# Performance work log

Measured on AMD Instinct MI355X. Metric: run time of the kernel, lower is better.

## Reference

```python
import jax, jax.numpy as jnp
import numpy as np

H = 16
D_MODEL = 1024
D_K = D_MODEL // H


def setup_inputs() -> dict:
    key = jax.random.key(0)
    ks = jax.random.split(key, 12)
    B, S = 4, 2048
    scale = 1.0 / np.sqrt(D_MODEL)
    inp = {
        "query": jax.random.normal(ks[0], (B, S, D_MODEL), dtype=jnp.float32),
        "key": jax.random.normal(ks[1], (B, S, D_MODEL), dtype=jnp.float32),
        "value": jax.random.normal(ks[2], (B, S, D_MODEL), dtype=jnp.float32),
        "Wq": jax.random.normal(ks[3], (D_MODEL, D_MODEL), dtype=jnp.float32) * scale,
        "bq": jnp.zeros((D_MODEL,), dtype=jnp.float32),
        "Wk": jax.random.normal(ks[4], (D_MODEL, D_MODEL), dtype=jnp.float32) * scale,
        "bk": jnp.zeros((D_MODEL,), dtype=jnp.float32),
        "Wv": jax.random.normal(ks[5], (D_MODEL, D_MODEL), dtype=jnp.float32) * scale,
        "bv": jnp.zeros((D_MODEL,), dtype=jnp.float32),
        "Wo": jax.random.normal(ks[6], (D_MODEL, D_MODEL), dtype=jnp.float32) * scale,
        "bo": jnp.zeros((D_MODEL,), dtype=jnp.float32),
    }
    return inp


def reference(query, key, value, Wq, bq, Wk, bk, Wv, bv, Wo, bo):
    B, S, _ = query.shape
    # Linear projections (torch Linear: x @ W^T + b), then split heads -> [B,H,S,d_k]
    def proj(x, W, b):
        y = x @ W.T + b
        return y.reshape(B, S, H, D_K).transpose(0, 2, 1, 3)

    q = proj(query, Wq, bq)
    k = proj(key, Wk, bk)
    v = proj(value, Wv, bv)

    # Explicit QK^T / sqrt(d_k), softmax, AV (no mask; dropout = identity in eval)
    scores = jnp.einsum("bhqd,bhkd->bhqk", q, k) / jnp.sqrt(jnp.float32(D_K))
    attn = jax.nn.softmax(scores, axis=-1)
    x = jnp.einsum("bhqk,bhkd->bhqd", attn, v)

    # Merge heads and final output projection
    x = x.transpose(0, 2, 1, 3).reshape(B, S, H * D_K)
    return x @ Wo.T + bo
```

## Files before the change

### kernel.cpp

```cpp
#include <hip/hip_runtime.h>
#include <hip/hip_bf16.h>
#include <stdint.h>

#define BATCH 4
#define SEQ   2048
#define DM    1024
#define NH    16
#define DK    64
#define MROWS (BATCH * SEQ)

#define C1 0.1803368801111204f

typedef __attribute__((ext_vector_type(8))) short short8;
typedef __attribute__((ext_vector_type(4))) float f32x4;
typedef __attribute__((ext_vector_type(4))) float floatv4;
typedef __attribute__((ext_vector_type(4))) unsigned short us4;
typedef __attribute__((ext_vector_type(4))) unsigned int uint4v;

static __device__ __forceinline__ unsigned short f2bf(float f) {
    union { float f; uint32_t u; } c; c.f = f;
    uint32_t u = c.u;
    return (unsigned short)((u + 0x7fffu + ((u >> 16) & 1u)) >> 16);
}

static __device__ __forceinline__ unsigned int cvt_pk_bf16(float a, float b) {
    __hip_bfloat162 h = __float22bfloat162_rn(float2{a, b});
    unsigned int u; __builtin_memcpy(&u, &h, 4); return u;
}

static __device__ __forceinline__ float ex2(float x) { return __builtin_amdgcn_exp2f(x); }

#define AS1C(p) ((const __attribute__((address_space(1))) unsigned int*)(uintptr_t)(const void*)(p))
#define AS3(p)  ((__attribute__((address_space(3))) unsigned int*)(uintptr_t)(void*)(p))

__global__ __launch_bounds__(256) void cvt3_k(const float* __restrict__ a, const float* __restrict__ b,
                                              const float* __restrict__ c,
                                              unsigned short* __restrict__ oa, unsigned short* __restrict__ ob,
                                              unsigned short* __restrict__ oc) {
    const int z = blockIdx.y;
    const float* s = (z == 0) ? a : (z == 1) ? b : c;
    unsigned short* o = (z == 0) ? oa : (z == 1) ? ob : oc;
    int i = blockIdx.x * 256 + threadIdx.x;
    floatv4 v = ((const floatv4*)s)[i];
    us4 w; w.x = f2bf(v.x); w.y = f2bf(v.y); w.z = f2bf(v.z); w.w = f2bf(v.w);
    ((us4*)o)[i] = w;
}

__global__ __launch_bounds__(256) void cvt4_k(const float* __restrict__ a, const float* __restrict__ b,
                                              const float* __restrict__ c, const float* __restrict__ d,
                                              unsigned short* __restrict__ oa, unsigned short* __restrict__ ob,
                                              unsigned short* __restrict__ oc, unsigned short* __restrict__ od) {
    const int z = blockIdx.y;
    const float* s = (z == 0) ? a : (z == 1) ? b : (z == 2) ? c : d;
    unsigned short* o = (z == 0) ? oa : (z == 1) ? ob : (z == 2) ? oc : od;
    int i = blockIdx.x * 256 + threadIdx.x;
    floatv4 v = ((const floatv4*)s)[i];
    us4 w; w.x = f2bf(v.x); w.y = f2bf(v.y); w.z = f2bf(v.z); w.w = f2bf(v.w);
    ((us4*)o)[i] = w;
}

template <int MODE>
static __device__ __forceinline__ void gemm_body(const unsigned short* __restrict__ A,
                                                 const unsigned short* __restrict__ Bw,
                                                 const float* __restrict__ bias,
                                                 void* __restrict__ out, int m0, int n0,
                                                 float scale) {
    const int tid = threadIdx.x;
    const int wave = tid >> 6, lane = tid & 63, quad = lane >> 4, l16 = lane & 15;
    const int wr = wave & 1, wc = wave >> 1;

    __shared__ alignas(16) unsigned short As[128 * 32];
    __shared__ alignas(16) unsigned short Bs[128 * 32];

    f32x4 acc[4][4];
    #pragma unroll
    for (int i = 0; i < 4; i++)
        #pragma unroll
        for (int j = 0; j < 4; j++) acc[i][j] = (f32x4){0.f, 0.f, 0.f, 0.f};

    const int srow = lane >> 2;
    const int scol = (lane & 3) * 8;

    for (int k0 = 0; k0 < DM; k0 += 32) {
        __syncthreads();
        #pragma unroll
        for (int t = 0; t < 2; t++) {
            const int rr = wave * 32 + t * 16;
            __builtin_amdgcn_global_load_lds(AS1C(A  + (size_t)(m0 + rr + srow) * DM + k0 + scol),
                                             AS3(&As[rr * 32]), 16, 0, 0);
            __builtin_amdgcn_global_load_lds(AS1C(Bw + (size_t)(n0 + rr + srow) * DM + k0 + scol),
                                             AS3(&Bs[rr * 32]), 16, 0, 0);
        }
        __syncthreads();

        short8 af[4], bf[4];
        #pragma unroll
        for (int i = 0; i < 4; i++) af[i] = *(const short8*)&As[(wr * 64 + i * 16 + l16) * 32 + quad * 8];
        #pragma unroll
        for (int i = 0; i < 4; i++) bf[i] = *(const short8*)&Bs[(wc * 64 + i * 16 + l16) * 32 + quad * 8];
        #pragma unroll
        for (int i = 0; i < 4; i++)
            #pragma unroll
            for (int j = 0; j < 4; j++)
                acc[i][j] = __builtin_amdgcn_mfma_f32_16x16x32_bf16(af[i], bf[j], acc[i][j], 0, 0, 0);
    }

    #pragma unroll
    for (int j = 0; j < 4; j++) {
        const int n = n0 + wc * 64 + j * 16 + l16;
        const float bv = bias[n];
        #pragma unroll
        for (int i = 0; i < 4; i++) {
            if (MODE == 2) {
                const int hh = n >> 6, dd = n & (DK - 1);
                const int bb = m0 >> 11;
                const size_t pos = (size_t)(m0 & (SEQ - 1))
                                 + (size_t)((wr * 2 + (i >> 1)) * 32 + quad * 8 + (i & 1) * 4);
                us4 w;
                #pragma unroll
                for (int r = 0; r < 4; r++) w[r] = f2bf(acc[i][j][r] + bv);
                *(us4*)((unsigned short*)out + (((size_t)bb * NH + hh) * DK + dd) * SEQ + pos) = w;
            } else {
                #pragma unroll
                for (int r = 0; r < 4; r++) {
                    const int mrow = m0 + wr * 64 + i * 16 + quad * 4 + r;
                    float val = (acc[i][j][r] + bv) * scale;
                    if (MODE == 0) {
                        int bb = mrow >> 11, ss = mrow & (SEQ - 1), hh = n >> 6, dd = n & (DK - 1);
                        ((unsigned short*)out)[((((size_t)bb * NH + hh) * SEQ + ss) << 6) + dd] = f2bf(val);
                    } else {
                        ((float*)out)[(size_t)mrow * DM + n] = val;
                    }
                }
            }
        }
    }
}

__global__ __launch_bounds__(256, 2) void gemm_qkv_k(const unsigned short* qa, const unsigned short* ka,
                                                     const unsigned short* va, const unsigned short* wq,
                                                     const unsigned short* wk, const unsigned short* wv,
                                                     const float* bq, const float* bk, const float* bv,
                                                     unsigned short* qh, unsigned short* kh, unsigned short* vtc) {
    const int z = blockIdx.z;
    if (z == 2) {
        gemm_body<2>(va, wv, bv, vtc, blockIdx.x * 128, blockIdx.y * 128, 1.0f);
    } else {
        const unsigned short* A = (z == 0) ? qa : ka;
        const unsigned short* W = (z == 0) ? wq : wk;
        const float* bi = (z == 0) ? bq : bk;
        unsigned short* o = (z == 0) ? qh : kh;
        const float sc = (z == 0) ? C1 : 1.0f;
        gemm_body<0>(A, W, bi, o, blockIdx.x * 128, blockIdx.y * 128, sc);
    }
}

__global__ __launch_bounds__(256, 2) void gemm_o_k(const unsigned short* xb, const unsigned short* wo,
                                                   const float* bo, float* out) {
    gemm_body<1>(xb, wo, bo, out, blockIdx.x * 128, blockIdx.y * 128, 1.0f);
}

__global__ __launch_bounds__(256, 4) void flash_attn_k(const unsigned short* __restrict__ Qh,
                                                       const unsigned short* __restrict__ Kh,
                                                       const unsigned short* __restrict__ Vtc,
                                                       unsigned short* __restrict__ Xb) {
    const int tid = threadIdx.x;
    const int wave = tid >> 6, lane = tid & 63, quad = lane >> 4, l16 = lane & 15;
    const int h = blockIdx.y, b = blockIdx.z;
    const unsigned short* Qp = Qh  + (size_t)(b * NH + h) * SEQ * DK;
    const unsigned short* Kp = Kh  + (size_t)(b * NH + h) * SEQ * DK;
    const unsigned short* Vp = Vtc + (size_t)(b * NH + h) * DK * SEQ;
    const int q0 = blockIdx.x * 128 + wave * 32;

    __shared__ alignas(16) unsigned short kt[128][72];
    __shared__ alignas(16) unsigned short vt[64][136];

    short8 aq[2][2];
    #pragma unroll
    for (int m = 0; m < 2; m++)
        #pragma unroll
        for (int kk = 0; kk < 2; kk++)
            aq[m][kk] = *(const short8*)(Qp + (size_t)(q0 + m * 16 + l16) * DK + kk * 32 + quad * 8);

    short8 ones;
    #pragma unroll
    for (int j = 0; j < 8; j++) ones[j] = (short)0x3F80;

    f32x4 O[2][4];
    f32x4 lacc[2];
    #pragma unroll
    for (int m = 0; m < 2; m++) {
        #pragma unroll
        for (int db = 0; db < 4; db++) O[m][db] = (f32x4){0.f, 0.f, 0.f, 0.f};
        lacc[m] = (f32x4){0.f, 0.f, 0.f, 0.f};
    }

    const unsigned short* kgp = Kp + (size_t)(tid >> 3) * DK + (tid & 7) * 8;
    const unsigned short* vgp = Vp + (size_t)(tid >> 4) * SEQ + (tid & 15) * 8;
    unsigned short* kws = &kt[tid >> 3][(tid & 7) * 8];
    unsigned short* vws = &vt[tid >> 4][(tid & 15) * 8];

    short8 krg[4], vrg[4];
    #pragma unroll
    for (int it = 0; it < 4; it++) {
        krg[it] = *(const short8*)(kgp + (size_t)it * 32 * DK);
        vrg[it] = *(const short8*)(vgp + (size_t)it * 16 * SEQ);
    }
    kgp += (size_t)128 * DK;
    vgp += 128;

    for (int t0 = 0; t0 < SEQ; t0 += 128) {
        __syncthreads();
        #pragma unroll
        for (int it = 0; it < 4; it++) {
            *(short8*)(kws + it * 32 * 72) = krg[it];
            *(short8*)(vws + it * 16 * 136) = vrg[it];
        }
        #pragma unroll
        for (int it = 0; it < 4; it++) {
            krg[it] = *(const short8*)(kgp + (size_t)it * 32 * DK);
            vrg[it] = *(const short8*)(vgp + (size_t)it * 16 * SEQ);
        }
        kgp += (size_t)128 * DK;
        vgp += 128;
        asm volatile("s_waitcnt lgkmcnt(0)" ::: "memory");
        __builtin_amdgcn_s_barrier();
        __builtin_amdgcn_sched_barrier(0);

        #pragma unroll
        for (int t = 0; t < 4; t++) {
            f32x4 s[2][2];
            #pragma unroll
            for (int m = 0; m < 2; m++)
                #pragma unroll
                for (int sb = 0; sb < 2; sb++) s[m][sb] = (f32x4){0.f, 0.f, 0.f, 0.f};

            #pragma unroll
            for (int kk = 0; kk < 2; kk++) {
                short8 bk0 = *(const short8*)&kt[(t * 2    ) * 16 + l16][kk * 32 + quad * 8];
                short8 bk1 = *(const short8*)&kt[(t * 2 + 1) * 16 + l16][kk * 32 + quad * 8];
                s[0][0] = __builtin_amdgcn_mfma_f32_16x16x32_bf16(bk0, aq[0][kk], s[0][0], 0, 0, 0);
                s[0][1] = __builtin_amdgcn_mfma_f32_16x16x32_bf16(bk1, aq[0][kk], s[0][1], 0, 0, 0);
                s[1][0] = __builtin_amdgcn_mfma_f32_16x16x32_bf16(bk0, aq[1][kk], s[1][0], 0, 0, 0);
                s[1][1] = __builtin_amdgcn_mfma_f32_16x16x32_bf16(bk1, aq[1][kk], s[1][1], 0, 0, 0);
            }

            short8 pa[2];
            #pragma unroll
            for (int m = 0; m < 2; m++) {
                uint4v pk;
                pk.x = cvt_pk_bf16(ex2(s[m][0][0]), ex2(s[m][0][1]));
                pk.y = cvt_pk_bf16(ex2(s[m][0][2]), ex2(s[m][0][3]));
                pk.z = cvt_pk_bf16(ex2(s[m][1][0]), ex2(s[m][1][1]));
                pk.w = cvt_pk_bf16(ex2(s[m][1][2]), ex2(s[m][1][3]));
                __builtin_memcpy(&pa[m], &pk, 16);
            }

            #pragma unroll
            for (int db = 0; db < 4; db++) {
                short8 vf = *(const short8*)&vt[db * 16 + l16][t * 32 + quad * 8];
                O[0][db] = __builtin_amdgcn_mfma_f32_16x16x32_bf16(pa[0], vf, O[0][db], 0, 0, 0);
                O[1][db] = __builtin_amdgcn_mfma_f32_16x16x32_bf16(pa[1], vf, O[1][db], 0, 0, 0);
            }
            lacc[0] = __builtin_amdgcn_mfma_f32_16x16x32_bf16(pa[0], ones, lacc[0], 0, 0, 0);
            lacc[1] = __builtin_amdgcn_mfma_f32_16x16x32_bf16(pa[1], ones, lacc[1], 0, 0, 0);
        }
    }

    #pragma unroll
    for (int m = 0; m < 2; m++) {
        #pragma unroll
        for (int r = 0; r < 4; r++) {
            const float inv = 1.f / lacc[m][r];
            const int srow = q0 + m * 16 + quad * 4 + r;
            unsigned short* op = Xb + ((size_t)b * SEQ + srow) * DM + h * DK;
            #pragma unroll
            for (int db = 0; db < 4; db++)
                op[db * 16 + l16] = f2bf(O[m][db][r] * inv);
        }
    }
}

extern "C" void kernel_launch(void* const* d_in, const int* in_sizes, int n_in,
                              void* d_out, int out_size, void* d_ws, size_t ws_size,
                              hipStream_t stream) {
    const float* q_in = (const float*)d_in[0];
    const float* k_in = (const float*)d_in[1];
    const float* v_in = (const float*)d_in[2];
    const float* Wq   = (const float*)d_in[3];
    const float* bq   = (const float*)d_in[4];
    const float* Wk   = (const float*)d_in[5];
    const float* bk   = (const float*)d_in[6];
    const float* Wv   = (const float*)d_in[7];
    const float* bv   = (const float*)d_in[8];
    const float* Wo   = (const float*)d_in[9];
    const float* bo   = (const float*)d_in[10];

    const size_t MB = 1024ull * 1024ull;
    char* ws = (char*)d_ws;
    unsigned short* qa  = (unsigned short*)(ws +   0 * MB);
    unsigned short* ka  = (unsigned short*)(ws +  16 * MB);
    unsigned short* va  = (unsigned short*)(ws +  32 * MB);
    unsigned short* wqb = (unsigned short*)(ws +  48 * MB);
    unsigned short* wkb = (unsigned short*)(ws +  50 * MB);
    unsigned short* wvb = (unsigned short*)(ws +  52 * MB);
    unsigned short* wob = (unsigned short*)(ws +  54 * MB);
    unsigned short* qh  = (unsigned short*)(ws +  56 * MB);
    unsigned short* kh  = (unsigned short*)(ws +  72 * MB);
    unsigned short* vtc = (unsigned short*)(ws +  88 * MB);
    unsigned short* xb  = (unsigned short*)(ws + 104 * MB);

    cvt3_k<<<dim3(8192, 3), 256, 0, stream>>>(q_in, k_in, v_in, qa, ka, va);
    cvt4_k<<<dim3(1024, 4), 256, 0, stream>>>(Wq, Wk, Wv, Wo, wqb, wkb, wvb, wob);

    gemm_qkv_k<<<dim3(MROWS / 128, DM / 128, 3), 256, 0, stream>>>(qa, ka, va, wqb, wkb, wvb,
                                                                   bq, bk, bv, qh, kh, vtc);

    flash_attn_k<<<dim3(SEQ / 128, NH, BATCH), 256, 0, stream>>>(qh, kh, vtc, xb);

    gemm_o_k<<<dim3(MROWS / 128, DM / 128), 256, 0, stream>>>(xb, wob, bo, (float*)d_out);
}
```

Before: 338.3 us.

## Replace projection GEMMs with 256x256-tile pipelined multi-buffered kernel

Rewrites the projection GEMM body to use 256x256 output tiles with 512 threads, a four-stage swizzled LDS buffer fed by async global-to-LDS loads, fine-grained vmcnt waits and MFMA priority hints, so loads overlap compute. The QKV launch is split into separate Q/K and V kernels, and the output projection uses the same body. It aims to raise arithmetic intensity and hide memory latency, at the cost of fewer blocks (one per CU) and more LDS and register pressure.

```diff
diff --git a/kernel.cpp b/kernel.cpp
--- a/kernel.cpp
+++ b/kernel.cpp
@@ -60,73 +60,136 @@
 }
 
 template <int MODE>
-static __device__ __forceinline__ void gemm_body(const unsigned short* __restrict__ A,
-                                                 const unsigned short* __restrict__ Bw,
-                                                 const float* __restrict__ bias,
-                                                 void* __restrict__ out, int m0, int n0,
-                                                 float scale) {
+static __device__ __forceinline__ void gemm256_body(const unsigned short* __restrict__ A,
+                                                    const unsigned short* __restrict__ Bw,
+                                                    const float* __restrict__ bias,
+                                                    void* __restrict__ out, int m0, int n0,
+                                                    float scale) {
+    constexpr int K = DM;
+    constexpr int NK = K / 64;
+    constexpr int NIT = NK / 2;
+
     const int tid = threadIdx.x;
     const int wave = tid >> 6, lane = tid & 63, quad = lane >> 4, l16 = lane & 15;
-    const int wr = wave & 1, wc = wave >> 1;
-
-    __shared__ alignas(16) unsigned short As[128 * 32];
-    __shared__ alignas(16) unsigned short Bs[128 * 32];
-
-    f32x4 acc[4][4];
-    #pragma unroll
-    for (int i = 0; i < 4; i++)
+    const int wm = wave >> 2, wn = wave & 3;
+
+    __shared__ alignas(16) unsigned short AsU[4 * 8192];
+    __shared__ alignas(16) unsigned short BsU[4 * 8192];
+
+    f32x4 acc[8][4];
+    #pragma unroll
+    for (int i = 0; i < 8; i++)
         #pragma unroll
         for (int j = 0; j < 4; j++) acc[i][j] = (f32x4){0.f, 0.f, 0.f, 0.f};
 
-    const int srow = lane >> 2;
-    const int scol = (lane & 3) * 8;
-
-    for (int k0 = 0; k0 < DM; k0 += 32) {
-        __syncthreads();
-        #pragma unroll
-        for (int t = 0; t < 2; t++) {
-            const int rr = wave * 32 + t * 16;
-            __builtin_amdgcn_global_load_lds(AS1C(A  + (size_t)(m0 + rr + srow) * DM + k0 + scol),
-                                             AS3(&As[rr * 32]), 16, 0, 0);
-            __builtin_amdgcn_global_load_lds(AS1C(Bw + (size_t)(n0 + rr + srow) * DM + k0 + scol),
-                                             AS3(&Bs[rr * 32]), 16, 0, 0);
-        }
-        __syncthreads();
-
-        short8 af[4], bf[4];
-        #pragma unroll
-        for (int i = 0; i < 4; i++) af[i] = *(const short8*)&As[(wr * 64 + i * 16 + l16) * 32 + quad * 8];
-        #pragma unroll
-        for (int i = 0; i < 4; i++) bf[i] = *(const short8*)&Bs[(wc * 64 + i * 16 + l16) * 32 + quad * 8];
-        #pragma unroll
-        for (int i = 0; i < 4; i++)
-            #pragma unroll
-            for (int j = 0; j < 4; j++)
-                acc[i][j] = __builtin_amdgcn_mfma_f32_16x16x32_bf16(af[i], bf[j], acc[i][j], 0, 0, 0);
-    }
-
-    #pragma unroll
-    for (int j = 0; j < 4; j++) {
-        const int n = n0 + wc * 64 + j * 16 + l16;
+    const int sl   = (lane & 7) ^ (lane >> 3);
+    const int grow = wave * 16 + (lane >> 3) * 2 + (sl >> 2);
+    const int gc8  = (sl & 3) * 8;
+    const unsigned short* Ag = A  + (size_t)(m0 + grow) * K + gc8;
+    const unsigned short* Bg = Bw + (size_t)(n0 + grow) * K + gc8;
+
+    const int sx8 = ((((l16 & 1) * 4 + quad) ^ (l16 >> 1)) * 8);
+    const int la  = wm * 4096 + (l16 >> 1) * 64 + sx8;
+    const int lb  = wn * 2048 + (l16 >> 1) * 64 + sx8;
+
+    short8 af[8], bfr[4];
+
+#define G256_STG(GP, LDSP, b, kh, kt)                                                     \
+    {   _Pragma("unroll")                                                                 \
+        for (int s_ = 0; s_ < 2; s_++)                                                    \
+            __builtin_amdgcn_global_load_lds(                                             \
+                AS1C(GP + (size_t)s_ * 128 * K + (kt) * 64 + (kh) * 32),                  \
+                AS3(LDSP + ((b) * 2 + (kh)) * 8192 + s_ * 4096 + wave * 512), 16, 0, 0); }
+
+#define G256_LD(b, kh)                                                                    \
+    {   const int rg_ = ((b) * 2 + (kh)) * 8192;                                          \
+        _Pragma("unroll")                                                                 \
+        for (int mf_ = 0; mf_ < 8; mf_++) af[mf_] = *(const short8*)&AsU[rg_ + la + mf_ * 512]; \
+        _Pragma("unroll")                                                                 \
+        for (int nf_ = 0; nf_ < 4; nf_++) bfr[nf_] = *(const short8*)&BsU[rg_ + lb + nf_ * 512]; }
+
+#define G256_MMA(nh)                                                                      \
+    {   __builtin_amdgcn_s_setprio(1);                                                    \
+        _Pragma("unroll")                                                                 \
+        for (int mf_ = 0; mf_ < 8; mf_++) {                                               \
+            acc[mf_][2*(nh)]   = __builtin_amdgcn_mfma_f32_16x16x32_bf16(af[mf_], bfr[2*(nh)],   acc[mf_][2*(nh)],   0, 0, 0); \
+            acc[mf_][2*(nh)+1] = __builtin_amdgcn_mfma_f32_16x16x32_bf16(af[mf_], bfr[2*(nh)+1], acc[mf_][2*(nh)+1], 0, 0, 0); } \
+        __builtin_amdgcn_s_setprio(0); }
+
+#define G256_VM10 asm volatile("s_waitcnt vmcnt(10)" ::: "memory")
+#define G256_VM0  asm volatile("s_waitcnt vmcnt(0)"  ::: "memory")
+#define G256_LG0  { asm volatile("s_waitcnt lgkmcnt(0)" ::: "memory"); __builtin_amdgcn_sched_barrier(0); }
+#define G256_BAR  __builtin_amdgcn_s_barrier()
+#define G256_SB0  __builtin_amdgcn_sched_barrier(0)
+
+    G256_STG(Ag, AsU, 0, 0, 0); G256_STG(Bg, BsU, 0, 0, 0);
+    G256_STG(Ag, AsU, 0, 1, 0); G256_STG(Bg, BsU, 0, 1, 0);
+    G256_STG(Ag, AsU, 1, 0, 1); G256_STG(Bg, BsU, 1, 0, 1);
+    G256_STG(Ag, AsU, 1, 1, 1);
+
+    #pragma unroll 1
+    for (int i = 0; i < NIT - 1; ++i) {
+        const int t2 = 2 * i + 2, t3 = 2 * i + 3;
+        G256_VM10; G256_BAR; G256_SB0;
+        G256_STG(Bg, BsU, 1, 1, 2 * i + 1);
+        G256_LD(0, 0); G256_LG0; G256_MMA(0); G256_BAR;
+        G256_STG(Ag, AsU, 0, 0, t2); G256_MMA(1);
+        G256_VM10; G256_BAR; G256_SB0;
+        G256_STG(Bg, BsU, 0, 0, t2);
+        G256_LD(0, 1); G256_LG0; G256_MMA(0); G256_BAR;
+        G256_STG(Ag, AsU, 0, 1, t2); G256_MMA(1);
+        G256_VM10; G256_BAR; G256_SB0;
+        G256_STG(Bg, BsU, 0, 1, t2);
+        G256_LD(1, 0); G256_LG0; G256_MMA(0); G256_BAR;
+        G256_STG(Ag, AsU, 1, 0, t3); G256_MMA(1);
+        G256_VM10; G256_BAR; G256_SB0;
+        G256_STG(Bg, BsU, 1, 0, t3);
+        G256_LD(1, 1); G256_LG0; G256_MMA(0); G256_BAR;
+        G256_STG(Ag, AsU, 1, 1, t3); G256_MMA(1);
+    }
+    G256_STG(Bg, BsU, 1, 1, NK - 1);
+    G256_VM0; G256_BAR; G256_SB0;
+    G256_LD(0, 0); G256_LG0; G256_MMA(0); G256_MMA(1);
+    G256_LD(0, 1); G256_LG0; G256_MMA(0); G256_MMA(1);
+    G256_LD(1, 0); G256_LG0; G256_MMA(0); G256_MMA(1);
+    G256_LD(1, 1); G256_LG0; G256_MMA(0); G256_MMA(1);
+
+#undef G256_STG
+#undef G256_LD
+#undef G256_MMA
+#undef G256_VM10
+#undef G256_VM0
+#undef G256_LG0
+#undef G256_BAR
+#undef G256_SB0
+
+    #pragma unroll
+    for (int nf = 0; nf < 4; nf++) {
+        const int n = n0 + wn * 64 + nf * 16 + l16;
         const float bv = bias[n];
-        #pragma unroll
-        for (int i = 0; i < 4; i++) {
-            if (MODE == 2) {
-                const int hh = n >> 6, dd = n & (DK - 1);
-                const int bb = m0 >> 11;
-                const size_t pos = (size_t)(m0 & (SEQ - 1))
-                                 + (size_t)((wr * 2 + (i >> 1)) * 32 + quad * 8 + (i & 1) * 4);
+        if (MODE == 2) {
+            const int bb = m0 >> 11;
+            const int hh = n >> 6, dd = n & (DK - 1);
+            unsigned short* obase = (unsigned short*)out
+                                  + (((size_t)bb * NH + hh) * DK + dd) * SEQ
+                                  + (m0 & (SEQ - 1)) + wm * 128 + quad * 8;
+            #pragma unroll
+            for (int mf = 0; mf < 8; mf++) {
                 us4 w;
                 #pragma unroll
-                for (int r = 0; r < 4; r++) w[r] = f2bf(acc[i][j][r] + bv);
-                *(us4*)((unsigned short*)out + (((size_t)bb * NH + hh) * DK + dd) * SEQ + pos) = w;
-            } else {
+                for (int r = 0; r < 4; r++) w[r] = f2bf(acc[mf][nf][r] + bv);
+                *(us4*)(obase + (mf >> 1) * 32 + (mf & 1) * 4) = w;
+            }
+        } else {
+            const int hh = n >> 6, dd = n & (DK - 1);
+            #pragma unroll
+            for (int mf = 0; mf < 8; mf++) {
                 #pragma unroll
                 for (int r = 0; r < 4; r++) {
-                    const int mrow = m0 + wr * 64 + i * 16 + quad * 4 + r;
-                    float val = (acc[i][j][r] + bv) * scale;
+                    const int mrow = m0 + wm * 128 + mf * 16 + quad * 4 + r;
+                    float val = (acc[mf][nf][r] + bv) * scale;
                     if (MODE == 0) {
-                        int bb = mrow >> 11, ss = mrow & (SEQ - 1), hh = n >> 6, dd = n & (DK - 1);
+                        int bb = mrow >> 11, ss = mrow & (SEQ - 1);
                         ((unsigned short*)out)[((((size_t)bb * NH + hh) * SEQ + ss) << 6) + dd] = f2bf(val);
                     } else {
                         ((float*)out)[(size_t)mrow * DM + n] = val;
@@ -137,27 +200,27 @@
     }
 }
 
-__global__ __launch_bounds__(256, 2) void gemm_qkv_k(const unsigned short* qa, const unsigned short* ka,
-                                                     const unsigned short* va, const unsigned short* wq,
-                                                     const unsigned short* wk, const unsigned short* wv,
-                                                     const float* bq, const float* bk, const float* bv,
-                                                     unsigned short* qh, unsigned short* kh, unsigned short* vtc) {
+__global__ __launch_bounds__(512, 1) void gemm_qk_k(const unsigned short* qa, const unsigned short* ka,
+                                                    const unsigned short* wq, const unsigned short* wk,
+                                                    const float* bq, const float* bk,
+                                                    unsigned short* qh, unsigned short* kh) {
     const int z = blockIdx.z;
-    if (z == 2) {
-        gemm_body<2>(va, wv, bv, vtc, blockIdx.x * 128, blockIdx.y * 128, 1.0f);
-    } else {
-        const unsigned short* A = (z == 0) ? qa : ka;
-        const unsigned short* W = (z == 0) ? wq : wk;
-        const float* bi = (z == 0) ? bq : bk;
-        unsigned short* o = (z == 0) ? qh : kh;
-        const float sc = (z == 0) ? C1 : 1.0f;
-        gemm_body<0>(A, W, bi, o, blockIdx.x * 128, blockIdx.y * 128, sc);
-    }
-}
-
-__global__ __launch_bounds__(256, 2) void gemm_o_k(const unsigned short* xb, const unsigned short* wo,
+    const unsigned short* A = (z == 0) ? qa : ka;
+    const unsigned short* W = (z == 0) ? wq : wk;
+    const float* bi = (z == 0) ? bq : bk;
+    unsigned short* o = (z == 0) ? qh : kh;
+    const float sc = (z == 0) ? C1 : 1.0f;
+    gemm256_body<0>(A, W, bi, o, blockIdx.x * 256, blockIdx.y * 256, sc);
+}
+
+__global__ __launch_bounds__(512, 1) void gemm_v_k(const unsigned short* va, const unsigned short* wv,
+                                                   const float* bv, unsigned short* vtc) {
+    gemm256_body<2>(va, wv, bv, vtc, blockIdx.x * 256, blockIdx.y * 256, 1.0f);
+}
+
+__global__ __launch_bounds__(512, 1) void gemm_o_k(const unsigned short* xb, const unsigned short* wo,
                                                    const float* bo, float* out) {
-    gemm_body<1>(xb, wo, bo, out, blockIdx.x * 128, blockIdx.y * 128, 1.0f);
+    gemm256_body<1>(xb, wo, bo, out, blockIdx.x * 256, blockIdx.y * 256, 1.0f);
 }
 
 __global__ __launch_bounds__(256, 4) void flash_attn_k(const unsigned short* __restrict__ Qh,
@@ -313,10 +376,11 @@
     cvt3_k<<<dim3(8192, 3), 256, 0, stream>>>(q_in, k_in, v_in, qa, ka, va);
     cvt4_k<<<dim3(1024, 4), 256, 0, stream>>>(Wq, Wk, Wv, Wo, wqb, wkb, wvb, wob);
 
-    gemm_qkv_k<<<dim3(MROWS / 128, DM / 128, 3), 256, 0, stream>>>(qa, ka, va, wqb, wkb, wvb,
-                                                                   bq, bk, bv, qh, kh, vtc);
+    gemm_qk_k<<<dim3(MROWS / 256, DM / 256, 2), 512, 0, stream>>>(qa, ka, wqb, wkb,
+                                                                  bq, bk, qh, kh);
+    gemm_v_k<<<dim3(MROWS / 256, DM / 256), 512, 0, stream>>>(va, wvb, bv, vtc);
 
     flash_attn_k<<<dim3(SEQ / 128, NH, BATCH), 256, 0, stream>>>(qh, kh, vtc, xb);
 
-    gemm_o_k<<<dim3(MROWS / 128, DM / 128), 256, 0, stream>>>(xb, wob, bo, (float*)d_out);
-}
+    gemm_o_k<<<dim3(MROWS / 256, DM / 256), 512, 0, stream>>>(xb, wob, bo, (float*)d_out);
+}
```

Result: slower. 349.4 us (+3.3%).
